# Performance work log

Measured on AMD Instinct MI355X. Metric: run time of the kernel, lower is better.

The kernel has to match this reference:

```python
import jax, jax.numpy as jnp
import numpy as np

E = 1024   # embedding_size
K = 64     # key_size
DH = 64    # head_size
H = 16     # layer_size (num heads)
F = 4096   # hidden_size
B, S = 4, 2048
EPS = float(np.finfo(np.float32).eps)  # torch RMSNorm default eps


def setup_inputs() -> dict:
    key = jax.random.key(0)
    ks = jax.random.split(key, 12)
    embeddings = jax.random.normal(ks[0], (B, S, E), dtype=jnp.float32)
    # causal additive mask: 0 on/below diagonal, -1e9 above
    tri = jnp.triu(jnp.ones((S, S), dtype=bool), k=1)
    causal_buffer = jnp.where(tri, -1e9, 0.0).astype(jnp.float32)[None]  # [1,S,S]
    # standard RoPE cos/sin buffers over the key dim
    inv_freq = 1.0 / (10000.0 ** (jnp.arange(0, K // 2, dtype=jnp.float32) * 2.0 / K))
    ang = jnp.arange(S, dtype=jnp.float32)[:, None] * inv_freq[None, :]  # [S,K/2]
    ang = jnp.concatenate([ang, ang], axis=-1)                           # [S,K]
    cos_buffer = jnp.cos(ang)[None]  # [1,S,K]
    sin_buffer = jnp.sin(ang)[None]
    sc = 0.02
    wq = jax.random.normal(ks[1], (H, E, K), dtype=jnp.float32) * sc
    wk = jax.random.normal(ks[2], (H, E, K), dtype=jnp.float32) * sc
    wv = jax.random.normal(ks[3], (H, E, DH), dtype=jnp.float32) * sc
    w_proj = jax.random.normal(ks[4], (E, E), dtype=jnp.float32) * sc
    attn_norm_w = jnp.ones((E,), dtype=jnp.float32)
    mlp_norm_w = jnp.ones((E,), dtype=jnp.float32)
    w_up = jax.random.normal(ks[5], (E, F), dtype=jnp.float32) * sc
    w_gate = jax.random.normal(ks[6], (E, F), dtype=jnp.float32) * sc
    w_down = jax.random.normal(ks[7], (F, E), dtype=jnp.float32) * sc
    return {"embeddings": embeddings, "causal_buffer": causal_buffer,
            "cos_buffer": cos_buffer, "sin_buffer": sin_buffer,
            "wq": wq, "wk": wk, "wv": wv, "w_proj": w_proj,
            "attn_norm_w": attn_norm_w, "mlp_norm_w": mlp_norm_w,
            "w_up": w_up, "w_gate": w_gate, "w_down": w_down}


def _rmsnorm(x, w):
    ms = jnp.mean(x * x, axis=-1, keepdims=True)
    return x * jax.lax.rsqrt(ms + EPS) * w


def _rotate(x, cos, sin):
    # x: [B,H,S,K]; cos/sin: [1,1,S,K]. swapped = cat(second_half, first_half)
    swapped = jnp.concatenate([x[..., K // 2:], x[..., :K // 2]], axis=-1)
    return cos * x + sin * swapped


def reference(embeddings, causal_buffer, cos_buffer, sin_buffer,
              wq, wk, wv, w_proj, attn_norm_w, mlp_norm_w,
              w_up, w_gate, w_down):
    cos = cos_buffer[:, None]  # [1,1,S,K]
    sin = sin_buffer[:, None]
    # NOTE: original computes attention_norm(embeddings) but feeds RAW
    # embeddings to the heads; we reproduce that faithfully.
    q = _rotate(jnp.einsum('bse,hek->bhsk', embeddings, wq), cos, sin)
    k = _rotate(jnp.einsum('bse,hek->bhsk', embeddings, wk), cos, sin)
    v = jnp.einsum('bse,hed->bhsd', embeddings, wv)
    scores = jnp.einsum('bhsk,bhtk->bhst', q, k) / jnp.sqrt(jnp.float32(K))
    scores = scores + causal_buffer[:, None]  # broadcast over heads
    weights = jax.nn.softmax(scores, axis=-1)
    attn = jnp.einsum('bhst,bhtd->bhsd', weights, v)  # [B,H,S,DH]
    attn = attn.transpose(0, 2, 1, 3).reshape(attn.shape[0], attn.shape[2], H * DH)
    x = embeddings + attn @ w_proj
    h = _rmsnorm(x, mlp_norm_w)
    mlp = (h @ w_up) * jax.nn.elu(h @ w_gate)
    return x + mlp @ w_down
```

## Files before the change

kernel.cpp:

```cpp
#include <hip/hip_runtime.h>
#include <cstdint>
#include <cstddef>

#define E_DIM 1024
#define S_LEN 2048
#define NB 4
#define NH 16
#define F_DIM 4096

typedef __attribute__((ext_vector_type(8))) __bf16 bf16x8;
typedef __attribute__((ext_vector_type(4))) __bf16 bf16x4;
typedef __attribute__((ext_vector_type(4))) float f32x4;
typedef __attribute__((ext_vector_type(16))) float f32x16;

__device__ __forceinline__ f32x4 mfma16(bf16x8 a, bf16x8 b, f32x4 c) {
  return __builtin_amdgcn_mfma_f32_16x16x32_bf16(a, b, c, 0, 0, 0);
}
__device__ __forceinline__ f32x16 mfma32(bf16x8 a, bf16x8 b, f32x16 c) {
  return __builtin_amdgcn_mfma_f32_32x32x16_bf16(a, b, c, 0, 0, 0);
}

__device__ __forceinline__ unsigned short f2bf(float f) {
  __bf16 h = (__bf16)f;
  return __builtin_bit_cast(unsigned short, h);
}

__device__ __forceinline__ void gl_lds16(const void* gptr, void* lptr) {
  __builtin_amdgcn_global_load_lds(
      (const __attribute__((address_space(1))) void*)gptr,
      (__attribute__((address_space(3))) void*)lptr, 16, 0, 0);
}


__global__ __launch_bounds__(256) void cast_emb_kernel(
    const float4* __restrict__ in, ushort4* __restrict__ out) {
  int i = blockIdx.x * 256 + threadIdx.x;
  float4 v = in[i];
  ushort4 o;
  o.x = f2bf(v.x); o.y = f2bf(v.y); o.z = f2bf(v.z); o.w = f2bf(v.w);
  out[i] = o;
}

__global__ __launch_bounds__(256) void transpose_cast_kernel(
    const float* __restrict__ in, unsigned short* __restrict__ out, int R, int C) {
  __shared__ float tile[32][33];
  const int bz = blockIdx.z;
  const float* ip = in + (size_t)bz * R * C;
  const int r0 = blockIdx.y * 32, c0 = blockIdx.x * 32;
  const int tc = threadIdx.x & 31, tr = threadIdx.x >> 5;
#pragma unroll
  for (int i = 0; i < 4; ++i)
    tile[tr + i * 8][tc] = ip[(size_t)(r0 + tr + i * 8) * C + (c0 + tc)];
  __syncthreads();
#pragma unroll
  for (int i = 0; i < 4; ++i)
    out[(size_t)(bz * C + c0 + tr + i * 8) * R + (r0 + tc)] = f2bf(tile[tc][tr + i * 8]);
}

__global__ __launch_bounds__(256) void transpose_cast_qkv(
    const float* __restrict__ wq, const float* __restrict__ wk,
    const float* __restrict__ wv, unsigned short* __restrict__ out) {
  __shared__ float tile[32][33];
  const int bz = blockIdx.z;
  const int which = bz >> 4, hz = bz & 15;
  const float* ip =
      (which == 0 ? wq : which == 1 ? wk : wv) + (size_t)hz * 1024 * 64;
  unsigned short* op = out + (size_t)which * 1024 * 1024;
  const int r0 = blockIdx.y * 32, c0 = blockIdx.x * 32;
  const int tc = threadIdx.x & 31, tr = threadIdx.x >> 5;
#pragma unroll
  for (int i = 0; i < 4; ++i)
    tile[tr + i * 8][tc] = ip[(size_t)(r0 + tr + i * 8) * 64 + (c0 + tc)];
  __syncthreads();
#pragma unroll
  for (int i = 0; i < 4; ++i)
    op[(size_t)(hz * 64 + c0 + tr + i * 8) * 1024 + (r0 + tc)] =
        f2bf(tile[tc][tr + i * 8]);
}

__global__ __launch_bounds__(256) void transpose_cast_upgate(
    const float* __restrict__ wup, const float* __restrict__ wgate,
    unsigned short* __restrict__ out) {
  __shared__ float tile[32][33];
  const int z = blockIdx.z & 1;
  const float* ip = z ? wgate : wup;
  const int r0 = blockIdx.y * 32, c0 = blockIdx.x * 32;
  const int tc = threadIdx.x & 31, tr = threadIdx.x >> 5;
#pragma unroll
  for (int i = 0; i < 4; ++i)
    tile[tr + i * 8][tc] = ip[(size_t)(r0 + tr + i * 8) * F_DIM + (c0 + tc)];
  __syncthreads();
#pragma unroll
  for (int i = 0; i < 4; ++i) {
    const int c = c0 + tr + i * 8;
    const int row = 64 * (c >> 5) + (c & 31) + z * 32;
    out[(size_t)row * E_DIM + (r0 + tc)] = f2bf(tile[tc][tr + i * 8]);
  }
}

template <int EPI, int KD>
__global__ __launch_bounds__(256) void gemm_bt(
    const unsigned short* __restrict__ A, const unsigned short* __restrict__ Bt,
    const float* __restrict__ aux, const float* __restrict__ cosb,
    const float* __restrict__ sinb,
    unsigned short* __restrict__ qout, unsigned short* __restrict__ kout,
    unsigned short* __restrict__ vtout, float* __restrict__ fout,
    unsigned short* __restrict__ gout) {
  __shared__ unsigned short As[128 * 64];
  __shared__ unsigned short Bs[128 * 64];
  const int t = threadIdx.x;
  const int lane = t & 63, w = t >> 6;
  const int l31 = lane & 31, half = lane >> 5;
  const int wm = (w >> 1) * 64, wn = (w & 1) * 64;
  const int m0 = blockIdx.y * 128, n0 = blockIdx.x * 128;
  const int sr = t >> 3, sc = t & 7;
  const int gcoff = (sc ^ (sr & 7)) * 8;
  const unsigned short* ga = A + (size_t)(m0 + sr) * KD + gcoff;
  const unsigned short* gb = Bt + (size_t)(n0 + sr) * KD + gcoff;
  unsigned short* lA = &As[sr * 64 + sc * 8];
  unsigned short* lB = &Bs[sr * 64 + sc * 8];
  const int xh = lane & 7;
  f32x16 acc[2][2] = {};
  for (int k0 = 0; k0 < KD; k0 += 64) {
    __syncthreads();
#pragma unroll
    for (int i = 0; i < 4; ++i) {
      gl_lds16(ga + (size_t)(i * 32) * KD + k0, lA + i * 32 * 64);
      gl_lds16(gb + (size_t)(i * 32) * KD + k0, lB + i * 32 * 64);
    }
    __syncthreads();
#pragma unroll
    for (int ksl = 0; ksl < 4; ++ksl) {
      const int cp = ((ksl * 2 + half) ^ xh) * 8;
      bf16x8 af[2], bfr[2];
#pragma unroll
      for (int mi = 0; mi < 2; ++mi)
        af[mi] = *reinterpret_cast<const bf16x8*>(&As[(wm + mi * 32 + l31) * 64 + cp]);
#pragma unroll
      for (int ni = 0; ni < 2; ++ni)
        bfr[ni] = *reinterpret_cast<const bf16x8*>(&Bs[(wn + ni * 32 + l31) * 64 + cp]);
#pragma unroll
      for (int mi = 0; mi < 2; ++mi)
#pragma unroll
        for (int ni = 0; ni < 2; ++ni)
          acc[mi][ni] = mfma32(af[mi], bfr[ni], acc[mi][ni]);
    }
  }
  if (EPI == 0) {
#pragma unroll
    for (int mi = 0; mi < 2; ++mi)
#pragma unroll
      for (int ni = 0; ni < 2; ++ni) {
        const int n = n0 + wn + ni * 32 + l31;
        const int seg = n >> 10, rest = n & 1023, hh = rest >> 6, kk = rest & 63;
#pragma unroll
        for (int reg = 0; reg < 16; ++reg) {
          const int m = m0 + wm + mi * 32 + (reg & 3) + 8 * (reg >> 2) + 4 * half;
          const int b = m >> 11, s = m & 2047;
          const float v = acc[mi][ni][reg];
          if (seg == 2) {
            vtout[(((size_t)(b * NH + hh)) * 64 + kk) * S_LEN + s] = f2bf(v);
          } else {
            const float sw = acc[mi][ni ^ 1][reg];
            const float cv = cosb[s * 64 + kk], sv = sinb[s * 64 + kk];
            const float scl = (seg == 0) ? 0.125f : 1.0f;
            unsigned short* dst = (seg == 0) ? qout : kout;
            dst[(((size_t)(b * NH + hh)) * S_LEN + s) * 64 + kk] =
                f2bf((cv * v + sv * sw) * scl);
          }
        }
      }
  } else if (EPI == 3) {
    const int col = ((n0 + wn) >> 1) + l31;
#pragma unroll
    for (int mi = 0; mi < 2; ++mi)
#pragma unroll
      for (int reg = 0; reg < 16; ++reg) {
        const int m = m0 + wm + mi * 32 + (reg & 3) + 8 * (reg >> 2) + 4 * half;
        const float u = acc[mi][0][reg], gt = acc[mi][1][reg];
        const float e = gt > 0.f ? gt : (__expf(gt) - 1.f);
        gout[(size_t)m * F_DIM + col] = f2bf(u * e);
      }
  } else {
#pragma unroll
    for (int mi = 0; mi < 2; ++mi)
#pragma unroll
      for (int ni = 0; ni < 2; ++ni) {
        const int n = n0 + wn + ni * 32 + l31;
#pragma unroll
        for (int reg = 0; reg < 16; ++reg) {
          const int m = m0 + wm + mi * 32 + (reg & 3) + 8 * (reg >> 2) + 4 * half;
          const size_t idx = (size_t)m * 1024 + n;
          fout[idx] = aux[idx] + acc[mi][ni][reg];
        }
      }
  }
}

#define PS_STRIDE 68
__global__ __launch_bounds__(256) void flash_attn(
    const unsigned short* __restrict__ qb, const unsigned short* __restrict__ kb,
    const unsigned short* __restrict__ vtb, unsigned short* __restrict__ attn) {
  __shared__ unsigned short Ks[64 * 64];
  __shared__ unsigned short Vts[64 * 64];
  __shared__ unsigned short Ps[128 * PS_STRIDE];
  const int t = threadIdx.x, lane = t & 63, w = t >> 6;
  const int quad = lane >> 4, l15 = lane & 15;
  const int qt = 15 - blockIdx.y;
  const int bh = blockIdx.x;
  const int b = bh >> 4, hh = bh & 15;
  const unsigned short* qg = qb + (size_t)bh * S_LEN * 64;
  const unsigned short* kg = kb + (size_t)bh * S_LEN * 64;
  const unsigned short* vg = vtb + (size_t)bh * 64 * S_LEN;
  bf16x8 aq[2][2];
#pragma unroll
  for (int mi = 0; mi < 2; ++mi)
#pragma unroll
    for (int ks = 0; ks < 2; ++ks)
      aq[mi][ks] = *reinterpret_cast<const bf16x8*>(
          qg + (size_t)(qt * 128 + w * 32 + mi * 16 + l15) * 64 + ks * 32 + quad * 8);
  f32x4 o[2][4] = {};
  float lpart[2][4] = {};
  const int srk = t >> 3, sck = t & 7;
  const int gck = ((sck ^ (srk & 7)) * 8);
  const int xh = l15 & 7;
  const int ktmax = 2 * qt + 1;
  for (int kt = 0; kt <= ktmax; ++kt) {
    __syncthreads();
#pragma unroll
    for (int i = 0; i < 2; ++i) {
      gl_lds16(kg + (size_t)(kt * 64 + srk + i * 32) * 64 + gck,
               &Ks[(srk + i * 32) * 64 + sck * 8]);
      gl_lds16(vg + (size_t)(srk + i * 32) * S_LEN + kt * 64 + gck,
               &Vts[(srk + i * 32) * 64 + sck * 8]);
    }
    __syncthreads();
    f32x4 sacc[2][4];
#pragma unroll
    for (int mi = 0; mi < 2; ++mi)
#pragma unroll
      for (int nt = 0; nt < 4; ++nt) sacc[mi][nt] = (f32x4){-8.f, -8.f, -8.f, -8.f};
#pragma unroll
    for (int nt = 0; nt < 4; ++nt) {
      bf16x8 b0 = *reinterpret_cast<const bf16x8*>(
          &Ks[(nt * 16 + l15) * 64 + ((quad ^ xh) * 8)]);
      bf16x8 b1 = *reinterpret_cast<const bf16x8*>(
          &Ks[(nt * 16 + l15) * 64 + (((4 + quad) ^ xh) * 8)]);
#pragma unroll
      for (int mi = 0; mi < 2; ++mi) {
        sacc[mi][nt] = mfma16(aq[mi][0], b0, sacc[mi][nt]);
        sacc[mi][nt] = mfma16(aq[mi][1], b1, sacc[mi][nt]);
      }
    }
    if (kt >= 2 * qt) {
#pragma unroll
      for (int mi = 0; mi < 2; ++mi)
#pragma unroll
        for (int nt = 0; nt < 4; ++nt)
#pragma unroll
          for (int rg = 0; rg < 4; ++rg) {
            const int row = qt * 128 + w * 32 + mi * 16 + quad * 4 + rg;
            const int col = kt * 64 + nt * 16 + l15;
            if (col > row) sacc[mi][nt][rg] = -1e9f;
          }
    }
#pragma unroll
    for (int mi = 0; mi < 2; ++mi)
#pragma unroll
      for (int nt = 0; nt < 4; ++nt)
#pragma unroll
        for (int rg = 0; rg < 4; ++rg) {
          const float p = __expf(sacc[mi][nt][rg]);
          lpart[mi][rg] += p;
          Ps[(w * 32 + mi * 16 + quad * 4 + rg) * PS_STRIDE + nt * 16 + l15] = f2bf(p);
        }
#pragma unroll
    for (int ks = 0; ks < 2; ++ks) {
      bf16x8 ap[2];
#pragma unroll
      for (int mi = 0; mi < 2; ++mi) {
        const unsigned short* pp =
            &Ps[(w * 32 + mi * 16 + l15) * PS_STRIDE + ks * 32 + quad * 8];
        bf16x4 lo = *reinterpret_cast<const bf16x4*>(pp);
        bf16x4 hi = *reinterpret_cast<const bf16x4*>(pp + 4);
        ap[mi] = __builtin_shufflevector(lo, hi, 0, 1, 2, 3, 4, 5, 6, 7);
      }
#pragma unroll
      for (int vt = 0; vt < 4; ++vt) {
        bf16x8 bv = *reinterpret_cast<const bf16x8*>(
            &Vts[(vt * 16 + l15) * 64 + (((ks * 4 + quad) ^ xh) * 8)]);
#pragma unroll
        for (int mi = 0; mi < 2; ++mi) o[mi][vt] = mfma16(ap[mi], bv, o[mi][vt]);
      }
    }
  }
  float linv[2][4];
#pragma unroll
  for (int mi = 0; mi < 2; ++mi)
#pragma unroll
    for (int rg = 0; rg < 4; ++rg) {
      float rs = lpart[mi][rg];
#pragma unroll
      for (int d = 1; d < 16; d <<= 1) rs += __shfl_xor(rs, d);
      linv[mi][rg] = 1.0f / rs;
    }
#pragma unroll
  for (int mi = 0; mi < 2; ++mi)
#pragma unroll
    for (int vt = 0; vt < 4; ++vt)
#pragma unroll
      for (int rg = 0; rg < 4; ++rg) {
        const int row = w * 32 + mi * 16 + quad * 4 + rg;
        const int s = qt * 128 + row;
        const float ov = o[mi][vt][rg] * linv[mi][rg];
        attn[((size_t)(b * S_LEN + s)) * E_DIM + hh * 64 + vt * 16 + l15] = f2bf(ov);
      }
}

__global__ __launch_bounds__(256) void rmsnorm_kernel(
    const float* __restrict__ x, const float* __restrict__ wgt,
    unsigned short* __restrict__ hout) {
  const int row = blockIdx.x;
  const int t = threadIdx.x;
  const float4 v = reinterpret_cast<const float4*>(x + (size_t)row * E_DIM)[t];
  float ss = v.x * v.x + v.y * v.y + v.z * v.z + v.w * v.w;
#pragma unroll
  for (int d = 1; d < 64; d <<= 1) ss += __shfl_xor(ss, d);
  __shared__ float red[4];
  if ((t & 63) == 0) red[t >> 6] = ss;
  __syncthreads();
  const float tot = red[0] + red[1] + red[2] + red[3];
  const float sc = rsqrtf(tot * (1.f / 1024.f) + 1.1920929e-07f);
  const float4 g = reinterpret_cast<const float4*>(wgt)[t];
  ushort4 ov;
  ov.x = f2bf(v.x * sc * g.x);
  ov.y = f2bf(v.y * sc * g.y);
  ov.z = f2bf(v.z * sc * g.z);
  ov.w = f2bf(v.w * sc * g.w);
  reinterpret_cast<ushort4*>(hout + (size_t)row * E_DIM)[t] = ov;
}

extern "C" void kernel_launch(void* const* d_in, const int* in_sizes, int n_in,
                              void* d_out, int out_size, void* d_ws, size_t ws_size,
                              hipStream_t stream) {
  (void)in_sizes; (void)n_in; (void)out_size; (void)ws_size;
  const float* emb = (const float*)d_in[0];
  const float* cosb = (const float*)d_in[2];
  const float* sinb = (const float*)d_in[3];
  const float* wq = (const float*)d_in[4];
  const float* wk = (const float*)d_in[5];
  const float* wv = (const float*)d_in[6];
  const float* wproj = (const float*)d_in[7];
  const float* mlpw = (const float*)d_in[9];
  const float* wup = (const float*)d_in[10];
  const float* wgate = (const float*)d_in[11];
  const float* wdown = (const float*)d_in[12];
  float* out = (float*)d_out;
  char* ws = (char*)d_ws;
  unsigned short* wqkv_t = (unsigned short*)(ws + 0);
  unsigned short* wproj_t = (unsigned short*)(ws + 6291456);
  unsigned short* wupgate_t = (unsigned short*)(ws + 8388608);
  unsigned short* wdown_t = (unsigned short*)(ws + 25165824);
  unsigned short* embb = (unsigned short*)(ws + 33554432);
  unsigned short* qbuf = (unsigned short*)(ws + 50331648);
  unsigned short* kbuf = (unsigned short*)(ws + 67108864);
  unsigned short* vtbuf = (unsigned short*)(ws + 83886080);
  unsigned short* gbuf = (unsigned short*)(ws + 33554432);
  unsigned short* attnb = (unsigned short*)(ws + 100663296);
  float* xbuf = (float*)(ws + 117440512);
  unsigned short* hbuf = (unsigned short*)(ws + 150994944);

  dim3 blk(256);
  cast_emb_kernel<<<8192, blk, 0, stream>>>((const float4*)emb, (ushort4*)embb);
  transpose_cast_qkv<<<dim3(2, 32, 48), blk, 0, stream>>>(wq, wk, wv, wqkv_t);
  transpose_cast_kernel<<<dim3(32, 32, 1), blk, 0, stream>>>(wproj, wproj_t, 1024, 1024);
  transpose_cast_upgate<<<dim3(128, 32, 2), blk, 0, stream>>>(wup, wgate, wupgate_t);
  transpose_cast_kernel<<<dim3(32, 128, 1), blk, 0, stream>>>(wdown, wdown_t, 4096, 1024);
  gemm_bt<0, 1024><<<dim3(24, 64), blk, 0, stream>>>(
      embb, wqkv_t, nullptr, cosb, sinb, qbuf, kbuf, vtbuf, nullptr, nullptr);
  flash_attn<<<dim3(64, 16), blk, 0, stream>>>(qbuf, kbuf, vtbuf, attnb);
  gemm_bt<1, 1024><<<dim3(8, 64), blk, 0, stream>>>(
      attnb, wproj_t, emb, nullptr, nullptr, nullptr, nullptr, nullptr, xbuf, nullptr);
  rmsnorm_kernel<<<8192, blk, 0, stream>>>(xbuf, mlpw, hbuf);
  gemm_bt<3, 1024><<<dim3(64, 64), blk, 0, stream>>>(
      hbuf, wupgate_t, nullptr, nullptr, nullptr, nullptr, nullptr, nullptr, nullptr, gbuf);
  gemm_bt<2, 4096><<<dim3(8, 64), blk, 0, stream>>>(
      gbuf, wdown_t, xbuf, nullptr, nullptr, nullptr, nullptr, nullptr, out, nullptr);
}
```

Baseline: 629.5 us.

## Split-K the down-projection GEMM with atomic accumulation and adjust LDS swizzle

The down-projection GEMM (K=4096) now runs as a 2-way split-K over a z grid dimension. Each half atomically adds its partial results into the output, which is first initialised with the residual through a device-to-device memcpy. This doubles the block count (512 to 1024) to fill more CUs on a GEMM that previously had few tiles. The LDS swizzle also gains an extra XOR term that flips the chunk index for rows 16-31 of each 32-row group, a change aimed at bank conflicts. In exchange the output moves from plain stores to fp32 atomics, which adds extra memory traffic and makes the summation order nondeterministic.

```diff
diff --git a/kernel.cpp b/kernel.cpp
--- a/kernel.cpp
+++ b/kernel.cpp
@@ -98,7 +98,7 @@
   }
 }
 
-template <int EPI, int KD>
+template <int EPI, int KD, int KSTR>
 __global__ __launch_bounds__(256) void gemm_bt(
     const unsigned short* __restrict__ A, const unsigned short* __restrict__ Bt,
     const float* __restrict__ aux, const float* __restrict__ cosb,
@@ -113,20 +113,21 @@
   const int l31 = lane & 31, half = lane >> 5;
   const int wm = (w >> 1) * 64, wn = (w & 1) * 64;
   const int m0 = blockIdx.y * 128, n0 = blockIdx.x * 128;
+  const int kz = blockIdx.z * KD;
   const int sr = t >> 3, sc = t & 7;
-  const int gcoff = (sc ^ (sr & 7)) * 8;
-  const unsigned short* ga = A + (size_t)(m0 + sr) * KD + gcoff;
-  const unsigned short* gb = Bt + (size_t)(n0 + sr) * KD + gcoff;
+  const int gcoff = ((sc ^ (sr & 7) ^ ((sr >> 2) & 4)) * 8);
+  const unsigned short* ga = A + (size_t)(m0 + sr) * KSTR + kz + gcoff;
+  const unsigned short* gb = Bt + (size_t)(n0 + sr) * KSTR + kz + gcoff;
   unsigned short* lA = &As[sr * 64 + sc * 8];
   unsigned short* lB = &Bs[sr * 64 + sc * 8];
-  const int xh = lane & 7;
+  const int xh = (lane & 7) ^ ((lane >> 2) & 4);
   f32x16 acc[2][2] = {};
   for (int k0 = 0; k0 < KD; k0 += 64) {
     __syncthreads();
 #pragma unroll
     for (int i = 0; i < 4; ++i) {
-      gl_lds16(ga + (size_t)(i * 32) * KD + k0, lA + i * 32 * 64);
-      gl_lds16(gb + (size_t)(i * 32) * KD + k0, lB + i * 32 * 64);
+      gl_lds16(ga + (size_t)(i * 32) * KSTR + k0, lA + i * 32 * 64);
+      gl_lds16(gb + (size_t)(i * 32) * KSTR + k0, lB + i * 32 * 64);
     }
     __syncthreads();
 #pragma unroll
@@ -180,6 +181,18 @@
         const float u = acc[mi][0][reg], gt = acc[mi][1][reg];
         const float e = gt > 0.f ? gt : (__expf(gt) - 1.f);
         gout[(size_t)m * F_DIM + col] = f2bf(u * e);
+      }
+  } else if (EPI == 4) {
+#pragma unroll
+    for (int mi = 0; mi < 2; ++mi)
+#pragma unroll
+      for (int ni = 0; ni < 2; ++ni) {
+        const int n = n0 + wn + ni * 32 + l31;
+#pragma unroll
+        for (int reg = 0; reg < 16; ++reg) {
+          const int m = m0 + wm + mi * 32 + (reg & 3) + 8 * (reg >> 2) + 4 * half;
+          atomicAdd(&fout[(size_t)m * 1024 + n], acc[mi][ni][reg]);
+        }
       }
   } else {
 #pragma unroll
@@ -376,14 +389,15 @@
   transpose_cast_kernel<<<dim3(32, 32, 1), blk, 0, stream>>>(wproj, wproj_t, 1024, 1024);
   transpose_cast_upgate<<<dim3(128, 32, 2), blk, 0, stream>>>(wup, wgate, wupgate_t);
   transpose_cast_kernel<<<dim3(32, 128, 1), blk, 0, stream>>>(wdown, wdown_t, 4096, 1024);
-  gemm_bt<0, 1024><<<dim3(24, 64), blk, 0, stream>>>(
+  gemm_bt<0, 1024, 1024><<<dim3(24, 64), blk, 0, stream>>>(
       embb, wqkv_t, nullptr, cosb, sinb, qbuf, kbuf, vtbuf, nullptr, nullptr);
   flash_attn<<<dim3(64, 16), blk, 0, stream>>>(qbuf, kbuf, vtbuf, attnb);
-  gemm_bt<1, 1024><<<dim3(8, 64), blk, 0, stream>>>(
+  gemm_bt<1, 1024, 1024><<<dim3(8, 64), blk, 0, stream>>>(
       attnb, wproj_t, emb, nullptr, nullptr, nullptr, nullptr, nullptr, xbuf, nullptr);
   rmsnorm_kernel<<<8192, blk, 0, stream>>>(xbuf, mlpw, hbuf);
-  gemm_bt<3, 1024><<<dim3(64, 64), blk, 0, stream>>>(
+  gemm_bt<3, 1024, 1024><<<dim3(64, 64), blk, 0, stream>>>(
       hbuf, wupgate_t, nullptr, nullptr, nullptr, nullptr, nullptr, nullptr, nullptr, gbuf);
-  gemm_bt<2, 4096><<<dim3(8, 64), blk, 0, stream>>>(
-      gbuf, wdown_t, xbuf, nullptr, nullptr, nullptr, nullptr, nullptr, out, nullptr);
-}
+  hipMemcpyAsync(out, xbuf, (size_t)8192 * 1024 * 4, hipMemcpyDeviceToDevice, stream);
+  gemm_bt<4, 2048, 4096><<<dim3(8, 64, 2), blk, 0, stream>>>(
+      gbuf, wdown_t, nullptr, nullptr, nullptr, nullptr, nullptr, nullptr, out, nullptr);
+}
```

Measured after the change: 672.8 us. +6.9%, slower.

## Double-buffer K/V tiles in flash attention and use 64-row tiles for narrow GEMMs

Applied to the files above, without the earlier changes.

Flash attention now keeps two LDS buffers for K and V^T and prefetches the next key tile while computing on the current one, removing one barrier per iteration. This is meant to hide global-to-LDS latency behind MFMA work. The GEMM kernel gains an M-tile template parameter, and the projection and down GEMMs (N=1024) use 64-row tiles to double block count and improve CU occupancy across the GPU. The costs are extra LDS in attention, less reuse of B tiles in the narrow GEMMs, and reliance on the single barrier to order async loads.

```diff
diff --git a/kernel.cpp b/kernel.cpp
--- a/kernel.cpp
+++ b/kernel.cpp
@@ -98,7 +98,7 @@
   }
 }
 
-template <int EPI, int KD>
+template <int EPI, int KD, int MT>
 __global__ __launch_bounds__(256) void gemm_bt(
     const unsigned short* __restrict__ A, const unsigned short* __restrict__ Bt,
     const float* __restrict__ aux, const float* __restrict__ cosb,
@@ -106,13 +106,14 @@
     unsigned short* __restrict__ qout, unsigned short* __restrict__ kout,
     unsigned short* __restrict__ vtout, float* __restrict__ fout,
     unsigned short* __restrict__ gout) {
-  __shared__ unsigned short As[128 * 64];
+  constexpr int MI = MT / 64;
+  __shared__ unsigned short As[MT * 64];
   __shared__ unsigned short Bs[128 * 64];
   const int t = threadIdx.x;
   const int lane = t & 63, w = t >> 6;
   const int l31 = lane & 31, half = lane >> 5;
-  const int wm = (w >> 1) * 64, wn = (w & 1) * 64;
-  const int m0 = blockIdx.y * 128, n0 = blockIdx.x * 128;
+  const int wm = (w >> 1) * (MT / 2), wn = (w & 1) * 64;
+  const int m0 = blockIdx.y * MT, n0 = blockIdx.x * 128;
   const int sr = t >> 3, sc = t & 7;
   const int gcoff = (sc ^ (sr & 7)) * 8;
   const unsigned short* ga = A + (size_t)(m0 + sr) * KD + gcoff;
@@ -120,27 +121,28 @@
   unsigned short* lA = &As[sr * 64 + sc * 8];
   unsigned short* lB = &Bs[sr * 64 + sc * 8];
   const int xh = lane & 7;
-  f32x16 acc[2][2] = {};
+  f32x16 acc[MI][2] = {};
   for (int k0 = 0; k0 < KD; k0 += 64) {
     __syncthreads();
 #pragma unroll
-    for (int i = 0; i < 4; ++i) {
+    for (int i = 0; i < MT / 32; ++i)
       gl_lds16(ga + (size_t)(i * 32) * KD + k0, lA + i * 32 * 64);
+#pragma unroll
+    for (int i = 0; i < 4; ++i)
       gl_lds16(gb + (size_t)(i * 32) * KD + k0, lB + i * 32 * 64);
-    }
     __syncthreads();
 #pragma unroll
     for (int ksl = 0; ksl < 4; ++ksl) {
       const int cp = ((ksl * 2 + half) ^ xh) * 8;
-      bf16x8 af[2], bfr[2];
-#pragma unroll
-      for (int mi = 0; mi < 2; ++mi)
+      bf16x8 af[MI], bfr[2];
+#pragma unroll
+      for (int mi = 0; mi < MI; ++mi)
         af[mi] = *reinterpret_cast<const bf16x8*>(&As[(wm + mi * 32 + l31) * 64 + cp]);
 #pragma unroll
       for (int ni = 0; ni < 2; ++ni)
         bfr[ni] = *reinterpret_cast<const bf16x8*>(&Bs[(wn + ni * 32 + l31) * 64 + cp]);
 #pragma unroll
-      for (int mi = 0; mi < 2; ++mi)
+      for (int mi = 0; mi < MI; ++mi)
 #pragma unroll
         for (int ni = 0; ni < 2; ++ni)
           acc[mi][ni] = mfma32(af[mi], bfr[ni], acc[mi][ni]);
@@ -148,7 +150,7 @@
   }
   if (EPI == 0) {
 #pragma unroll
-    for (int mi = 0; mi < 2; ++mi)
+    for (int mi = 0; mi < MI; ++mi)
 #pragma unroll
       for (int ni = 0; ni < 2; ++ni) {
         const int n = n0 + wn + ni * 32 + l31;
@@ -173,7 +175,7 @@
   } else if (EPI == 3) {
     const int col = ((n0 + wn) >> 1) + l31;
 #pragma unroll
-    for (int mi = 0; mi < 2; ++mi)
+    for (int mi = 0; mi < MI; ++mi)
 #pragma unroll
       for (int reg = 0; reg < 16; ++reg) {
         const int m = m0 + wm + mi * 32 + (reg & 3) + 8 * (reg >> 2) + 4 * half;
@@ -183,7 +185,7 @@
       }
   } else {
 #pragma unroll
-    for (int mi = 0; mi < 2; ++mi)
+    for (int mi = 0; mi < MI; ++mi)
 #pragma unroll
       for (int ni = 0; ni < 2; ++ni) {
         const int n = n0 + wn + ni * 32 + l31;
@@ -201,8 +203,8 @@
 __global__ __launch_bounds__(256) void flash_attn(
     const unsigned short* __restrict__ qb, const unsigned short* __restrict__ kb,
     const unsigned short* __restrict__ vtb, unsigned short* __restrict__ attn) {
-  __shared__ unsigned short Ks[64 * 64];
-  __shared__ unsigned short Vts[64 * 64];
+  __shared__ unsigned short Ks[2][64 * 64];
+  __shared__ unsigned short Vts[2][64 * 64];
   __shared__ unsigned short Ps[128 * PS_STRIDE];
   const int t = threadIdx.x, lane = t & 63, w = t >> 6;
   const int quad = lane >> 4, l15 = lane & 15;
@@ -225,16 +227,24 @@
   const int gck = ((sck ^ (srk & 7)) * 8);
   const int xh = l15 & 7;
   const int ktmax = 2 * qt + 1;
+#pragma unroll
+  for (int i = 0; i < 2; ++i) {
+    gl_lds16(kg + (size_t)(srk + i * 32) * 64 + gck, &Ks[0][(srk + i * 32) * 64 + sck * 8]);
+    gl_lds16(vg + (size_t)(srk + i * 32) * S_LEN + gck, &Vts[0][(srk + i * 32) * 64 + sck * 8]);
+  }
   for (int kt = 0; kt <= ktmax; ++kt) {
+    const int cur = kt & 1;
     __syncthreads();
-#pragma unroll
-    for (int i = 0; i < 2; ++i) {
-      gl_lds16(kg + (size_t)(kt * 64 + srk + i * 32) * 64 + gck,
-               &Ks[(srk + i * 32) * 64 + sck * 8]);
-      gl_lds16(vg + (size_t)(srk + i * 32) * S_LEN + kt * 64 + gck,
-               &Vts[(srk + i * 32) * 64 + sck * 8]);
-    }
-    __syncthreads();
+    if (kt < ktmax) {
+      const int nk = kt + 1;
+#pragma unroll
+      for (int i = 0; i < 2; ++i) {
+        gl_lds16(kg + (size_t)(nk * 64 + srk + i * 32) * 64 + gck,
+                 &Ks[cur ^ 1][(srk + i * 32) * 64 + sck * 8]);
+        gl_lds16(vg + (size_t)(srk + i * 32) * S_LEN + nk * 64 + gck,
+                 &Vts[cur ^ 1][(srk + i * 32) * 64 + sck * 8]);
+      }
+    }
     f32x4 sacc[2][4];
 #pragma unroll
     for (int mi = 0; mi < 2; ++mi)
@@ -243,9 +253,9 @@
 #pragma unroll
     for (int nt = 0; nt < 4; ++nt) {
       bf16x8 b0 = *reinterpret_cast<const bf16x8*>(
-          &Ks[(nt * 16 + l15) * 64 + ((quad ^ xh) * 8)]);
+          &Ks[cur][(nt * 16 + l15) * 64 + ((quad ^ xh) * 8)]);
       bf16x8 b1 = *reinterpret_cast<const bf16x8*>(
-          &Ks[(nt * 16 + l15) * 64 + (((4 + quad) ^ xh) * 8)]);
+          &Ks[cur][(nt * 16 + l15) * 64 + (((4 + quad) ^ xh) * 8)]);
 #pragma unroll
       for (int mi = 0; mi < 2; ++mi) {
         sacc[mi][nt] = mfma16(aq[mi][0], b0, sacc[mi][nt]);
@@ -288,7 +298,7 @@
 #pragma unroll
       for (int vt = 0; vt < 4; ++vt) {
         bf16x8 bv = *reinterpret_cast<const bf16x8*>(
-            &Vts[(vt * 16 + l15) * 64 + (((ks * 4 + quad) ^ xh) * 8)]);
+            &Vts[cur][(vt * 16 + l15) * 64 + (((ks * 4 + quad) ^ xh) * 8)]);
 #pragma unroll
         for (int mi = 0; mi < 2; ++mi) o[mi][vt] = mfma16(ap[mi], bv, o[mi][vt]);
       }
@@ -376,14 +386,14 @@
   transpose_cast_kernel<<<dim3(32, 32, 1), blk, 0, stream>>>(wproj, wproj_t, 1024, 1024);
   transpose_cast_upgate<<<dim3(128, 32, 2), blk, 0, stream>>>(wup, wgate, wupgate_t);
   transpose_cast_kernel<<<dim3(32, 128, 1), blk, 0, stream>>>(wdown, wdown_t, 4096, 1024);
-  gemm_bt<0, 1024><<<dim3(24, 64), blk, 0, stream>>>(
+  gemm_bt<0, 1024, 128><<<dim3(24, 64), blk, 0, stream>>>(
       embb, wqkv_t, nullptr, cosb, sinb, qbuf, kbuf, vtbuf, nullptr, nullptr);
   flash_attn<<<dim3(64, 16), blk, 0, stream>>>(qbuf, kbuf, vtbuf, attnb);
-  gemm_bt<1, 1024><<<dim3(8, 64), blk, 0, stream>>>(
+  gemm_bt<1, 1024, 64><<<dim3(8, 128), blk, 0, stream>>>(
       attnb, wproj_t, emb, nullptr, nullptr, nullptr, nullptr, nullptr, xbuf, nullptr);
   rmsnorm_kernel<<<8192, blk, 0, stream>>>(xbuf, mlpw, hbuf);
-  gemm_bt<3, 1024><<<dim3(64, 64), blk, 0, stream>>>(
+  gemm_bt<3, 1024, 128><<<dim3(64, 64), blk, 0, stream>>>(
       hbuf, wupgate_t, nullptr, nullptr, nullptr, nullptr, nullptr, nullptr, nullptr, gbuf);
-  gemm_bt<2, 4096><<<dim3(8, 64), blk, 0, stream>>>(
+  gemm_bt<2, 4096, 64><<<dim3(8, 128), blk, 0, stream>>>(
       gbuf, wdown_t, xbuf, nullptr, nullptr, nullptr, nullptr, nullptr, out, nullptr);
 }
```

New measurement: 673.9 us. +7.1%, slower.
